# Kernel optimization log

Measured on AMD Instinct MI355X. Metric: run time of the kernel, lower is better.

## Reference

```python
import jax, jax.numpy as jnp
import numpy as np
from jax import lax

B, T, D = 4, 8192, 1024


def setup_inputs() -> dict:
    key = jax.random.key(0)
    ks = jax.random.split(key, 8)
    x = jax.random.randint(ks[0], (B, T), 0, 256)
    embed = jax.random.normal(ks[1], (256, D), dtype=jnp.float32) * 0.02
    conv_w = jax.random.normal(ks[2], (D, D, 4), dtype=jnp.float32) / np.sqrt(4 * D)
    conv_b = jnp.zeros((D,), jnp.float32)
    ln_g = jnp.ones((D,), jnp.float32)
    ln_b = jnp.zeros((D,), jnp.float32)
    # matches torch init: log(exp(randn*0.1) - 1e-6)
    log_lambda = jnp.log(jnp.exp(jax.random.normal(ks[3], (D,), dtype=jnp.float32) * 0.1) - 1e-6)
    bW = jax.random.normal(ks[4], (D, D), dtype=jnp.float32) / np.sqrt(D)
    bb = jnp.zeros((D,), jnp.float32)
    cW = jax.random.normal(ks[5], (D, D), dtype=jnp.float32) / np.sqrt(D)
    cb = jnp.zeros((D,), jnp.float32)
    return dict(x=x, embed=embed, conv_w=conv_w, conv_b=conv_b, ln_g=ln_g,
                ln_b=ln_b, log_lambda=log_lambda, bW=bW, bb=bb, cW=cW, cb=cb)


def _forward(x, embed, conv_w, conv_b, ln_g, ln_b, log_lambda, bW, bb, cW, cb):
    h = embed[x]                                  # [B, T, D]
    # Conv1d(k=4, stride=4, pad=0) == non-overlapping patch GEMM
    xr = h.reshape(B, T // 4, 4, D)               # [B, T/4, 4, D]
    y = jnp.einsum('btkd,odk->bto', xr, conv_w) + conv_b  # [B, T/4, D]
    # LayerNorm (eps=1e-5, torch default)
    mu = jnp.mean(y, axis=-1, keepdims=True)
    var = jnp.mean((y - mu) ** 2, axis=-1, keepdims=True)
    y = (y - mu) * lax.rsqrt(var + 1e-5) * ln_g + ln_b
    # SimpleSSM (LRU)
    lam = jax.nn.sigmoid(jnp.exp(log_lambda))     # [D]
    xb = jnp.einsum('btd,od->bto', y, bW) + bb    # [B, T/4, D]

    def step(hc, xt):
        hn = lam * hc + (1.0 - lam) * xt
        return hn, hn

    h0 = jnp.zeros((B, D), y.dtype)
    _, hs = lax.scan(step, h0, xb.transpose(1, 0, 2))  # [T/4, B, D]
    h_all = hs.transpose(1, 0, 2)                 # [B, T/4, D]
    return jnp.einsum('btd,od->bto', h_all, cW) + cb


def reference(x, embed, conv_w, conv_b, ln_g, ln_b, log_lambda, bW, bb, cW, cb):
    return _forward(x, embed, conv_w, conv_b, ln_g, ln_b, log_lambda, bW, bb, cW, cb)
```

## Files before the change

### kernel.cpp

```cpp
#include <hip/hip_runtime.h>
#include <hip/hip_bf16.h>
#include <cstdint>


typedef __bf16 bf16;
typedef bf16 bf16x8 __attribute__((ext_vector_type(8)));
typedef bf16 bf16x4 __attribute__((ext_vector_type(4)));
typedef bf16 bf16x2 __attribute__((ext_vector_type(2)));
typedef float f32x4 __attribute__((ext_vector_type(4)));

#define TDIM   8192
#define TO     2048
#define D1K    1024

__device__ __forceinline__ void gload_lds16(const void* g, void* l) {
  __builtin_amdgcn_global_load_lds(
      (const __attribute__((address_space(1))) unsigned int*)(uintptr_t)g,
      (__attribute__((address_space(3))) unsigned int*)(uintptr_t)l,
      16, 0, 0);
}
__device__ __forceinline__ float bf2f(unsigned short u) {
  return __uint_as_float(((unsigned)u) << 16);
}

__global__ __launch_bounds__(256) void convert_w(
    const float* __restrict__ bW, const float* __restrict__ cW,
    const float* __restrict__ embed, const float* __restrict__ conv_w,
    bf16* __restrict__ bWb, bf16* __restrict__ cWb,
    bf16* __restrict__ embb, bf16* __restrict__ wkb) {
  int i = blockIdx.x * 256 + threadIdx.x;
  bWb[i] = (bf16)bW[i];
  cWb[i] = (bf16)cW[i];
  if (i < 256 * 1024) embb[i] = (bf16)embed[i];
  float4 cw = ((const float4*)conv_w)[i];
  wkb[0 * 1048576 + i] = (bf16)cw.x;
  wkb[1 * 1048576 + i] = (bf16)cw.y;
  wkb[2 * 1048576 + i] = (bf16)cw.z;
  wkb[3 * 1048576 + i] = (bf16)cw.w;
}

template <typename OutT>
__global__ __launch_bounds__(512) void gemm8(
    const bf16* __restrict__ A, const bf16* __restrict__ B,
    OutT* __restrict__ C, const float* __restrict__ bias,
    int M, int N, int K) {
  __shared__ bf16 sA[3][128 * 64];
  __shared__ bf16 sB[3][256 * 64];
  const int tid = threadIdx.x;
  const int lane = tid & 63, wave = tid >> 6;
  const int wm = wave >> 2, wn = wave & 3;
  const int m0 = blockIdx.x * 128, n0 = blockIdx.y * 256;
  const int kcnt = K >> 6;

  f32x4 acc[4][4] = {};

  auto stage = [&](int kt, int buf) {
    const int k0 = kt << 6;
#pragma unroll
    for (int c = 0; c < 2; ++c) {
      int p = c * 8192 + tid * 16;
      int row = p >> 7;
      int cs = ((p >> 4) & 7) ^ (row & 7);
      gload_lds16(A + (size_t)(m0 + row) * K + k0 + cs * 8,
                  &sA[buf][0] + c * 4096 + wave * 512);
    }
#pragma unroll
    for (int c = 0; c < 4; ++c) {
      int p = c * 8192 + tid * 16;
      int row = p >> 7;
      int cs = ((p >> 4) & 7) ^ (row & 7);
      gload_lds16(B + (size_t)(n0 + row) * K + k0 + cs * 8,
                  &sB[buf][0] + c * 4096 + wave * 512);
    }
  };

  stage(0, 0);
  stage(1, 1);

  int cur = 0;
  for (int kt = 0; kt < kcnt; ++kt) {
    if (kt + 1 < kcnt) {
      asm volatile("s_waitcnt vmcnt(6)" ::: "memory");
    } else {
      asm volatile("s_waitcnt vmcnt(0)" ::: "memory");
    }
    __builtin_amdgcn_s_barrier();
    if (kt + 2 < kcnt) {
      int nb = cur + 2; if (nb >= 3) nb -= 3;
      stage(kt + 2, nb);
    }

    const bf16* pA = &sA[cur][0];
    const bf16* pB = &sB[cur][0];
    const int g = lane >> 4;
    bf16x8 af[4][2], bfr[4][2];
#pragma unroll
    for (int i = 0; i < 4; ++i) {
      int ar = wm * 64 + i * 16 + (lane & 15);
#pragma unroll
      for (int ks = 0; ks < 2; ++ks)
        af[i][ks] = *(const bf16x8*)(pA + ar * 64 + (((ks << 2) | g) ^ (ar & 7)) * 8);
    }
#pragma unroll
    for (int j = 0; j < 4; ++j) {
      int br = wn * 64 + j * 16 + (lane & 15);
#pragma unroll
      for (int ks = 0; ks < 2; ++ks)
        bfr[j][ks] = *(const bf16x8*)(pB + br * 64 + (((ks << 2) | g) ^ (br & 7)) * 8);
    }
    __builtin_amdgcn_s_setprio(1);
#pragma unroll
    for (int ks = 0; ks < 2; ++ks)
#pragma unroll
      for (int i = 0; i < 4; ++i)
#pragma unroll
        for (int j = 0; j < 4; ++j)
          acc[i][j] = __builtin_amdgcn_mfma_f32_16x16x32_bf16(
              af[i][ks], bfr[j][ks], acc[i][j], 0, 0, 0);
    __builtin_amdgcn_s_setprio(0);
    cur += 1; if (cur >= 3) cur -= 3;
  }

#pragma unroll
  for (int i = 0; i < 4; ++i) {
    int mr = m0 + wm * 64 + i * 16 + (lane >> 4) * 4;
#pragma unroll
    for (int j = 0; j < 4; ++j) {
      int nc = n0 + wn * 64 + j * 16 + (lane & 15);
      float bv = bias ? bias[nc] : 0.0f;
#pragma unroll
      for (int r = 0; r < 4; ++r)
        C[(size_t)(mr + r) * N + nc] = (OutT)(acc[i][j][r] + bv);
    }
  }
}

__global__ __launch_bounds__(256) void gemm_btn64(
    const bf16* __restrict__ A, const bf16* __restrict__ B,
    bf16* __restrict__ C, int M, int N, int K) {
  constexpr int MF = 2, BM = 64;
  __shared__ bf16 sA[BM * 64];
  __shared__ bf16 sB[128 * 64];
  const int tid = threadIdx.x;
  const int lane = tid & 63, wave = tid >> 6;
  const int wm = wave >> 1, wn = wave & 1;
  const int m0 = blockIdx.x * BM, n0 = blockIdx.y * 128;

  f32x4 acc[MF][4] = {};

  const int kcnt = K >> 6;
  for (int kt = 0; kt < kcnt; ++kt) {
    const int k0 = kt << 6;
    __syncthreads();
#pragma unroll
    for (int i = 0; i < MF; ++i) {
      int p = i * 4096 + wave * 1024 + lane * 16;
      int row = p >> 7;
      int cs = ((p >> 4) & 7) ^ (row & 7);
      gload_lds16(A + (size_t)(m0 + row) * K + k0 + cs * 8,
                  sA + i * 2048 + wave * 512);
    }
#pragma unroll
    for (int i = 0; i < 4; ++i) {
      int p = i * 4096 + wave * 1024 + lane * 16;
      int row = p >> 7;
      int cs = ((p >> 4) & 7) ^ (row & 7);
      gload_lds16(B + (size_t)(n0 + row) * K + k0 + cs * 8,
                  sB + i * 2048 + wave * 512);
    }
    __syncthreads();

    const int g = lane >> 4;
    bf16x8 bfr[4][2];
#pragma unroll
    for (int f = 0; f < 4; ++f) {
      int br = wn * 64 + f * 16 + (lane & 15);
#pragma unroll
      for (int ks = 0; ks < 2; ++ks)
        bfr[f][ks] = *(const bf16x8*)(sB + br * 64 + (((ks << 2) | g) ^ (br & 7)) * 8);
    }
#pragma unroll
    for (int i = 0; i < MF; ++i) {
      int ar = wm * (MF * 16) + i * 16 + (lane & 15);
      bf16x8 a0 = *(const bf16x8*)(sA + ar * 64 + ((g) ^ (ar & 7)) * 8);
      bf16x8 a1 = *(const bf16x8*)(sA + ar * 64 + ((4 | g) ^ (ar & 7)) * 8);
#pragma unroll
      for (int j = 0; j < 4; ++j) {
        acc[i][j] = __builtin_amdgcn_mfma_f32_16x16x32_bf16(a0, bfr[j][0],
                                                            acc[i][j], 0, 0, 0);
        acc[i][j] = __builtin_amdgcn_mfma_f32_16x16x32_bf16(a1, bfr[j][1],
                                                            acc[i][j], 0, 0, 0);
      }
    }
  }
#pragma unroll
  for (int i = 0; i < MF; ++i) {
    int mr = m0 + wm * (MF * 16) + i * 16 + (lane >> 4) * 4;
#pragma unroll
    for (int j = 0; j < 4; ++j) {
      int nc = n0 + wn * 64 + j * 16 + (lane & 15);
#pragma unroll
      for (int r = 0; r < 4; ++r)
        C[(size_t)(mr + r) * N + nc] = (bf16)acc[i][j][r];
    }
  }
}

__global__ __launch_bounds__(256) void conv_ln(
    const int* __restrict__ x, const bf16* __restrict__ Mtab,
    const float* __restrict__ conv_b, const float* __restrict__ ln_g,
    const float* __restrict__ ln_b, bf16* __restrict__ yout) {
  const int tbase = blockIdx.x * 4;
  const int b = tbase >> 11;
  const int o4 = threadIdx.x;
  const float4 cb4 = ((const float4*)conv_b)[o4];
  const float4 g4 = ((const float4*)ln_g)[o4];
  const float4 b4 = ((const float4*)ln_b)[o4];
  const int lane = threadIdx.x & 63, wave = threadIdx.x >> 6;
  __shared__ float red[4][8];

  float y[4][4];
  float s[4], ss[4];
#pragma unroll
  for (int u = 0; u < 4; ++u) {
    const int t = tbase + u;
    const int to = t & 2047;
    const int4 xi = *(const int4*)(x + b * TDIM + to * 4);
    const bf16x4 a0 = *(const bf16x4*)(Mtab + (size_t)xi.x * 4096 +        o4 * 4);
    const bf16x4 a1 = *(const bf16x4*)(Mtab + (size_t)xi.y * 4096 + 1024 + o4 * 4);
    const bf16x4 a2 = *(const bf16x4*)(Mtab + (size_t)xi.z * 4096 + 2048 + o4 * 4);
    const bf16x4 a3 = *(const bf16x4*)(Mtab + (size_t)xi.w * 4096 + 3072 + o4 * 4);
    float y0 = (float)a0[0] + (float)a1[0] + (float)a2[0] + (float)a3[0] + cb4.x;
    float y1 = (float)a0[1] + (float)a1[1] + (float)a2[1] + (float)a3[1] + cb4.y;
    float y2 = (float)a0[2] + (float)a1[2] + (float)a2[2] + (float)a3[2] + cb4.z;
    float y3 = (float)a0[3] + (float)a1[3] + (float)a2[3] + (float)a3[3] + cb4.w;
    y[u][0] = y0; y[u][1] = y1; y[u][2] = y2; y[u][3] = y3;
    s[u] = y0 + y1 + y2 + y3;
    ss[u] = y0 * y0 + y1 * y1 + y2 * y2 + y3 * y3;
  }
#pragma unroll
  for (int off = 1; off < 64; off <<= 1) {
#pragma unroll
    for (int u = 0; u < 4; ++u) {
      s[u] += __shfl_xor(s[u], off);
      ss[u] += __shfl_xor(ss[u], off);
    }
  }
  if (lane == 0) {
#pragma unroll
    for (int u = 0; u < 4; ++u) { red[u][wave] = s[u]; red[u][wave + 4] = ss[u]; }
  }
  __syncthreads();
#pragma unroll
  for (int u = 0; u < 4; ++u) {
    const float sv = red[u][0] + red[u][1] + red[u][2] + red[u][3];
    const float sq = red[u][4] + red[u][5] + red[u][6] + red[u][7];
    const float mu = sv * (1.0f / 1024.0f);
    const float var = sq * (1.0f / 1024.0f) - mu * mu;
    const float rs = rsqrtf(var + 1e-5f);
    bf16x4 o;
    o[0] = (bf16)((y[u][0] - mu) * rs * g4.x + b4.x);
    o[1] = (bf16)((y[u][1] - mu) * rs * g4.y + b4.y);
    o[2] = (bf16)((y[u][2] - mu) * rs * g4.z + b4.z);
    o[3] = (bf16)((y[u][3] - mu) * rs * g4.w + b4.w);
    *(bf16x4*)(yout + (size_t)(tbase + u) * D1K + o4 * 4) = o;
  }
}

__global__ __launch_bounds__(256) void ssm_scan(
    const bf16* __restrict__ xb, const float* __restrict__ log_lambda,
    bf16* __restrict__ h_out) {
  const int bid = blockIdx.x;
  const int b = bid >> 6, c = (bid >> 1) & 31, half = bid & 1;
  const int d2 = half * 256 + threadIdx.x;
  const float e0 = expf(log_lambda[2 * d2]);
  const float e1 = expf(log_lambda[2 * d2 + 1]);
  const float l0 = 1.0f / (1.0f + expf(-e0));
  const float l1 = 1.0f / (1.0f + expf(-e1));
  const float o0 = 1.0f - l0, o1 = 1.0f - l1;
  const int tstart = c * 64;
  const int twarm = (tstart >= 48) ? tstart - 48 : 0;
  const ushort2* xp = (const ushort2*)(xb + ((size_t)b * TO + twarm) * D1K) + d2;
  float h0 = 0.0f, h1 = 0.0f;
  for (int t = twarm; t < tstart; ++t) {
    ushort2 v = *xp; xp += 512;
    h0 = l0 * h0 + o0 * bf2f(v.x);
    h1 = l1 * h1 + o1 * bf2f(v.y);
  }
  bf16x2* hp = (bf16x2*)(h_out + ((size_t)b * TO + tstart) * D1K) + d2;
#pragma unroll 4
  for (int t = 0; t < 64; ++t) {
    ushort2 v = *xp; xp += 512;
    h0 = l0 * h0 + o0 * bf2f(v.x);
    h1 = l1 * h1 + o1 * bf2f(v.y);
    bf16x2 o; o[0] = (bf16)h0; o[1] = (bf16)h1;
    *hp = o; hp += 512;
  }
}

extern "C" void kernel_launch(void* const* d_in, const int* in_sizes, int n_in,
                              void* d_out, int out_size, void* d_ws, size_t ws_size,
                              hipStream_t stream) {
  const int*   x      = (const int*)d_in[0];
  const float* embed  = (const float*)d_in[1];
  const float* conv_w = (const float*)d_in[2];
  const float* conv_b = (const float*)d_in[3];
  const float* ln_g   = (const float*)d_in[4];
  const float* ln_b   = (const float*)d_in[5];
  const float* log_l  = (const float*)d_in[6];
  const float* bW     = (const float*)d_in[7];
  const float* bb     = (const float*)d_in[8];
  const float* cW     = (const float*)d_in[9];
  const float* cb     = (const float*)d_in[10];
  float* out = (float*)d_out;
  char* ws = (char*)d_ws;

  bf16* Mtab = (bf16*)(ws + 0);
  bf16* bWb  = (bf16*)(ws + (2 << 20));
  bf16* cWb  = (bf16*)(ws + (4 << 20));
  bf16* embb = (bf16*)(ws + (6 << 20));
  bf16* wkb  = (bf16*)(ws + (6 << 20) + (512 << 10));
  bf16* yln  = (bf16*)(ws + (16 << 20));
  bf16* xbuf = (bf16*)(ws + (32 << 20));
  bf16* hb   = (bf16*)(ws + (48 << 20));

  convert_w<<<dim3(4096), dim3(256), 0, stream>>>(bW, cW, embed, conv_w,
                                                  bWb, cWb, embb, wkb);
  gemm_btn64<<<dim3(4, 32), dim3(256), 0, stream>>>(
      embb, wkb, Mtab, 256, 4096, 1024);
  conv_ln<<<dim3(2048), dim3(256), 0, stream>>>(x, Mtab, conv_b, ln_g, ln_b, yln);
  gemm8<bf16><<<dim3(64, 4), dim3(512), 0, stream>>>(
      yln, bWb, xbuf, bb, 8192, 1024, 1024);
  ssm_scan<<<dim3(256), dim3(256), 0, stream>>>(xbuf, log_l, hb);
  gemm8<float><<<dim3(64, 4), dim3(512), 0, stream>>>(
      hb, cWb, out, cb, 8192, 1024, 1024);
}
```

Baseline: 95.19 us.

## Pipeline small embed-conv GEMM with triple-buffered LDS and defer prefetch issue

Replaces the single-buffered, barrier-per-iteration gemm_btn64 with a triple-buffered gemm4p. It issues global-to-LDS loads two K-tiles ahead, waits on vmcnt instead of a full __syncthreads, and raises wave priority around the MFMA block. In both gemm8 and the new kernel, the prefetch for tile kt+2 now starts after the LDS fragment reads rather than before them, so the fragment reads are not delayed behind newly issued loads. This trades more LDS per block (three buffers) for overlap of memory latency with compute. The vmcnt(6) wait count must match the number of loads issued per stage.

```diff
diff --git a/kernel.cpp b/kernel.cpp
--- a/kernel.cpp
+++ b/kernel.cpp
@@ -85,10 +85,6 @@
       asm volatile("s_waitcnt vmcnt(0)" ::: "memory");
     }
     __builtin_amdgcn_s_barrier();
-    if (kt + 2 < kcnt) {
-      int nb = cur + 2; if (nb >= 3) nb -= 3;
-      stage(kt + 2, nb);
-    }
 
     const bf16* pA = &sA[cur][0];
     const bf16* pB = &sB[cur][0];
@@ -107,6 +103,10 @@
 #pragma unroll
       for (int ks = 0; ks < 2; ++ks)
         bfr[j][ks] = *(const bf16x8*)(pB + br * 64 + (((ks << 2) | g) ^ (br & 7)) * 8);
+    }
+    if (kt + 2 < kcnt) {
+      int nb = cur + 2; if (nb >= 3) nb -= 3;
+      stage(kt + 2, nb);
     }
     __builtin_amdgcn_s_setprio(1);
 #pragma unroll
@@ -135,67 +135,89 @@
   }
 }
 
-__global__ __launch_bounds__(256) void gemm_btn64(
+__global__ __launch_bounds__(256) void gemm4p(
     const bf16* __restrict__ A, const bf16* __restrict__ B,
     bf16* __restrict__ C, int M, int N, int K) {
-  constexpr int MF = 2, BM = 64;
-  __shared__ bf16 sA[BM * 64];
-  __shared__ bf16 sB[128 * 64];
+  __shared__ bf16 sA[3][64 * 64];
+  __shared__ bf16 sB[3][128 * 64];
   const int tid = threadIdx.x;
   const int lane = tid & 63, wave = tid >> 6;
   const int wm = wave >> 1, wn = wave & 1;
-  const int m0 = blockIdx.x * BM, n0 = blockIdx.y * 128;
-
-  f32x4 acc[MF][4] = {};
-
+  const int m0 = blockIdx.x * 64, n0 = blockIdx.y * 128;
   const int kcnt = K >> 6;
-  for (int kt = 0; kt < kcnt; ++kt) {
+
+  f32x4 acc[2][4] = {};
+
+  auto stage = [&](int kt, int buf) {
     const int k0 = kt << 6;
-    __syncthreads();
-#pragma unroll
-    for (int i = 0; i < MF; ++i) {
-      int p = i * 4096 + wave * 1024 + lane * 16;
+#pragma unroll
+    for (int c = 0; c < 2; ++c) {
+      int p = c * 4096 + tid * 16;
       int row = p >> 7;
       int cs = ((p >> 4) & 7) ^ (row & 7);
       gload_lds16(A + (size_t)(m0 + row) * K + k0 + cs * 8,
-                  sA + i * 2048 + wave * 512);
-    }
-#pragma unroll
-    for (int i = 0; i < 4; ++i) {
-      int p = i * 4096 + wave * 1024 + lane * 16;
+                  &sA[buf][0] + c * 2048 + wave * 512);
+    }
+#pragma unroll
+    for (int c = 0; c < 4; ++c) {
+      int p = c * 4096 + tid * 16;
       int row = p >> 7;
       int cs = ((p >> 4) & 7) ^ (row & 7);
       gload_lds16(B + (size_t)(n0 + row) * K + k0 + cs * 8,
-                  sB + i * 2048 + wave * 512);
-    }
-    __syncthreads();
-
+                  &sB[buf][0] + c * 2048 + wave * 512);
+    }
+  };
+
+  stage(0, 0);
+  stage(1, 1);
+
+  int cur = 0;
+  for (int kt = 0; kt < kcnt; ++kt) {
+    if (kt + 1 < kcnt) {
+      asm volatile("s_waitcnt vmcnt(6)" ::: "memory");
+    } else {
+      asm volatile("s_waitcnt vmcnt(0)" ::: "memory");
+    }
+    __builtin_amdgcn_s_barrier();
+
+    const bf16* pA = &sA[cur][0];
+    const bf16* pB = &sB[cur][0];
     const int g = lane >> 4;
-    bf16x8 bfr[4][2];
-#pragma unroll
-    for (int f = 0; f < 4; ++f) {
-      int br = wn * 64 + f * 16 + (lane & 15);
+    bf16x8 af[2][2], bfr[4][2];
+#pragma unroll
+    for (int i = 0; i < 2; ++i) {
+      int ar = wm * 32 + i * 16 + (lane & 15);
 #pragma unroll
       for (int ks = 0; ks < 2; ++ks)
-        bfr[f][ks] = *(const bf16x8*)(sB + br * 64 + (((ks << 2) | g) ^ (br & 7)) * 8);
-    }
-#pragma unroll
-    for (int i = 0; i < MF; ++i) {
-      int ar = wm * (MF * 16) + i * 16 + (lane & 15);
-      bf16x8 a0 = *(const bf16x8*)(sA + ar * 64 + ((g) ^ (ar & 7)) * 8);
-      bf16x8 a1 = *(const bf16x8*)(sA + ar * 64 + ((4 | g) ^ (ar & 7)) * 8);
-#pragma unroll
-      for (int j = 0; j < 4; ++j) {
-        acc[i][j] = __builtin_amdgcn_mfma_f32_16x16x32_bf16(a0, bfr[j][0],
-                                                            acc[i][j], 0, 0, 0);
-        acc[i][j] = __builtin_amdgcn_mfma_f32_16x16x32_bf16(a1, bfr[j][1],
-                                                            acc[i][j], 0, 0, 0);
-      }
-    }
-  }
-#pragma unroll
-  for (int i = 0; i < MF; ++i) {
-    int mr = m0 + wm * (MF * 16) + i * 16 + (lane >> 4) * 4;
+        af[i][ks] = *(const bf16x8*)(pA + ar * 64 + (((ks << 2) | g) ^ (ar & 7)) * 8);
+    }
+#pragma unroll
+    for (int j = 0; j < 4; ++j) {
+      int br = wn * 64 + j * 16 + (lane & 15);
+#pragma unroll
+      for (int ks = 0; ks < 2; ++ks)
+        bfr[j][ks] = *(const bf16x8*)(pB + br * 64 + (((ks << 2) | g) ^ (br & 7)) * 8);
+    }
+    if (kt + 2 < kcnt) {
+      int nb = cur + 2; if (nb >= 3) nb -= 3;
+      stage(kt + 2, nb);
+    }
+    __builtin_amdgcn_s_setprio(1);
+#pragma unroll
+    for (int ks = 0; ks < 2; ++ks)
+#pragma unroll
+      for (int i = 0; i < 2; ++i)
+#pragma unroll
+        for (int j = 0; j < 4; ++j)
+          acc[i][j] = __builtin_amdgcn_mfma_f32_16x16x32_bf16(
+              af[i][ks], bfr[j][ks], acc[i][j], 0, 0, 0);
+    __builtin_amdgcn_s_setprio(0);
+    cur += 1; if (cur >= 3) cur -= 3;
+  }
+
+#pragma unroll
+  for (int i = 0; i < 2; ++i) {
+    int mr = m0 + wm * 32 + i * 16 + (lane >> 4) * 4;
 #pragma unroll
     for (int j = 0; j < 4; ++j) {
       int nc = n0 + wn * 64 + j * 16 + (lane & 15);
@@ -326,7 +348,7 @@
 
   convert_w<<<dim3(4096), dim3(256), 0, stream>>>(bW, cW, embed, conv_w,
                                                   bWb, cWb, embb, wkb);
-  gemm_btn64<<<dim3(4, 32), dim3(256), 0, stream>>>(
+  gemm4p<<<dim3(4, 32), dim3(256), 0, stream>>>(
       embb, wkb, Mtab, 256, 4096, 1024);
   conv_ln<<<dim3(2048), dim3(256), 0, stream>>>(x, Mtab, conv_b, ln_g, ln_b, yln);
   gemm8<bf16><<<dim3(64, 4), dim3(512), 0, stream>>>(
```

After: 88.37 us. -7.2%, faster.
